# Kernel tuning notes

Measured on AMD Instinct MI355X. Metric: run time of the kernel, lower is better.

Reference implementation:

```python
import jax, jax.numpy as jnp
import numpy as np

H = 16  # number of heads

def setup_inputs() -> dict:
    key = jax.random.key(0)
    ks = jax.random.split(key, 8)
    B, T, D = 4, 2048, 1024
    s = 0.02
    return {
        "query": jax.random.normal(ks[0], (B, T, D), jnp.float32),
        "key":   jax.random.normal(ks[1], (B, T, D), jnp.float32),
        "value": jax.random.normal(ks[2], (B, T, D), jnp.float32),
        "mask":  jnp.ones((B, T, T), jnp.int32),
        # torch nn.Linear weights: [out_features, in_features]
        "Wq": jax.random.normal(ks[3], (D, D), jnp.float32) * s,
        "Wk": jax.random.normal(ks[4], (D, D), jnp.float32) * s,
        "Wv": jax.random.normal(ks[5], (D, D), jnp.float32) * s,
        "Wo": jax.random.normal(ks[6], (D, D), jnp.float32) * s,
        "bo": jnp.zeros((D,), jnp.float32),
    }

def reference(query, key, value, mask, Wq, Wk, Wv, Wo, bo):
    B, Tq, _ = query.shape
    Tk = key.shape[1]
    Dv = Wv.shape[0]
    # linear projections (y = x @ W^T), split into heads: [B, H, T, dh]
    Q = jnp.einsum('btd,ed->bte', query, Wq).reshape(B, Tq, H, -1).transpose(0, 2, 1, 3)
    K = jnp.einsum('btd,ed->bte', key,   Wk).reshape(B, Tk, H, -1).transpose(0, 2, 1, 3)
    V = jnp.einsum('btd,ed->bte', value, Wv).reshape(B, Tk, H, -1).transpose(0, 2, 1, 3)
    d_k = K.shape[-1]
    scores = jnp.einsum('bhqd,bhkd->bhqk', Q, K) / jnp.sqrt(jnp.asarray(d_k, Q.dtype))
    # mask broadcast: [B,1,Tq,Tk]; masked_fill(mask==0, -1e9)
    scores = jnp.where(mask[:, None] == 0, jnp.asarray(-1e9, scores.dtype), scores)
    attn = jax.nn.softmax(scores, axis=-1)
    Z = jnp.einsum('bhqk,bhkd->bhqd', attn, V)          # [B,H,Tq,dh]
    Zc = Z.transpose(0, 2, 1, 3).reshape(B, Tq, Dv)     # concat heads
    return jnp.einsum('btd,ed->bte', Zc, Wo) + bo
```

## Files before the change

kernel.cpp:

```cpp
#include <hip/hip_runtime.h>

typedef __bf16 bf16x8 __attribute__((ext_vector_type(8)));
typedef __bf16 bf16x4 __attribute__((ext_vector_type(4)));
typedef float f32x4 __attribute__((ext_vector_type(4)));
typedef unsigned short u16;
typedef unsigned long long u64;

#define NX 8388608
#define NW 1048576

__device__ __forceinline__ u16 f2bf(float f) {
  union { float f; unsigned u; } c; c.f = f;
  unsigned u = c.u;
  u += 0x7fffu + ((u >> 16) & 1u);
  return (u16)(u >> 16);
}

__device__ __forceinline__ f32x4 mfma16(bf16x8 a, bf16x8 b, f32x4 c) {
  return __builtin_amdgcn_mfma_f32_16x16x32_bf16(a, b, c, 0, 0, 0);
}

__device__ __forceinline__ void gld16(void* lds, const void* g) {
  __builtin_amdgcn_global_load_lds(
      (const __attribute__((address_space(1))) unsigned int*)g,
      (__attribute__((address_space(3))) unsigned int*)lds, 16, 0, 0);
}

__global__ __launch_bounds__(256) void cast_all(
    const float* __restrict__ q, const float* __restrict__ k,
    const float* __restrict__ v, const float* __restrict__ wq,
    const float* __restrict__ wk, const float* __restrict__ wv,
    const float* __restrict__ wo, u16* __restrict__ xbf, u16* __restrict__ wbf,
    const int* __restrict__ mask, u64* __restrict__ bits) {
  if (blockIdx.x >= 14336) {
    const int row = (blockIdx.x - 14336) * 4 + (threadIdx.x >> 6);
    const int lane = threadIdx.x & 63;
    const int* mrow = mask + (long long)row * 2048;
#pragma unroll
    for (int it = 0; it < 32; it++) {
      u64 w = __ballot(mrow[it * 64 + lane] != 0);
      if (lane == 0) bits[row * 32 + it] = w;
    }
    return;
  }
  long long i = ((long long)blockIdx.x * 256 + threadIdx.x) * 8;
  const float* src; u16* dst; long long off;
  if (i < (long long)NX)            { src = q; dst = xbf;            off = i; }
  else if (i < 2LL * NX)            { src = k; dst = xbf + NX;       off = i - NX; }
  else if (i < 3LL * NX)            { src = v; dst = xbf + 2LL * NX; off = i - 2LL * NX; }
  else {
    long long j = i - 3LL * NX;
    int w = (int)(j / NW); off = j - (long long)w * NW;
    src = (w == 0) ? wq : (w == 1) ? wk : (w == 2) ? wv : wo;
    dst = wbf + (long long)w * NW;
  }
  float4 a = *(const float4*)(src + off);
  float4 b = *(const float4*)(src + off + 4);
  u16 o[8] = {f2bf(a.x), f2bf(a.y), f2bf(a.z), f2bf(a.w),
              f2bf(b.x), f2bf(b.y), f2bf(b.z), f2bf(b.w)};
  *(uint4*)(dst + off) = *(const uint4*)o;
}

__device__ __forceinline__ void gstage(
    u16* sAb, u16* sBb, const u16* __restrict__ A, const u16* __restrict__ W,
    int m0, int n0, int k0, int wave, int lr, int gc) {
#pragma unroll
  for (int t = 0; t < 4; t++) {
    const int rb = wave * 32 + t * 8;
    gld16(&sAb[rb * 64], &A[(m0 + rb + lr) * 1024 + k0 + gc * 8]);
    gld16(&sBb[rb * 64], &W[(n0 + rb + lr) * 1024 + k0 + gc * 8]);
  }
}

template <int MODE>
__global__ __launch_bounds__(256, 2) void gemm128(
    const u16* __restrict__ Abase, const u16* __restrict__ Wbase,
    u16* __restrict__ oq, u16* __restrict__ ok, u16* __restrict__ ovt,
    const float* __restrict__ bias, float* __restrict__ of) {
  __shared__ alignas(16) u16 smem[2][2][128 * 64];
  const u16* A = Abase;
  const u16* W = Wbase;
  if (MODE == 0) { A += (long long)blockIdx.z * NX; W += (long long)blockIdx.z * NW; }
  const int tid = threadIdx.x, wave = tid >> 6, lane = tid & 63;
  const int quad = lane >> 4, l15 = lane & 15;
  const int id = blockIdx.y * 8 + blockIdx.x;
  const int id2 = (id & 7) * 64 + (id >> 3);
  const int m0 = (id2 >> 3) * 128, n0 = (id2 & 7) * 128;
  const int wm = (wave & 1) * 64, wn = (wave >> 1) * 64;
  const int lr = lane >> 3;
  const int gc = (lane & 7) ^ lr;
  f32x4 acc[4][4];
#pragma unroll
  for (int i = 0; i < 4; i++)
#pragma unroll
    for (int j = 0; j < 4; j++) acc[i][j] = (f32x4){0.f, 0.f, 0.f, 0.f};

  gstage(smem[0][0], smem[0][1], A, W, m0, n0, 0, wave, lr, gc);
  int buf = 0;
  for (int ks = 0; ks < 16; ks++) {
    if (ks < 15) {
      gstage(smem[buf ^ 1][0], smem[buf ^ 1][1], A, W, m0, n0, (ks + 1) * 64,
             wave, lr, gc);
      asm volatile("s_waitcnt vmcnt(8)" ::: "memory");
    } else {
      asm volatile("s_waitcnt vmcnt(0)" ::: "memory");
    }
    __builtin_amdgcn_s_barrier();
    __builtin_amdgcn_sched_barrier(0);
    const u16* cA = smem[buf][0];
    const u16* cB = smem[buf][1];
#pragma unroll
    for (int kc = 0; kc < 2; kc++) {
      bf16x8 aF[4], bF[4];
#pragma unroll
      for (int i = 0; i < 4; i++)
        aF[i] = *(const bf16x8*)&cA[(wm + 16 * i + l15) * 64 +
                                    (((kc * 4 + quad) ^ (l15 & 7)) * 8)];
#pragma unroll
      for (int j = 0; j < 4; j++)
        bF[j] = *(const bf16x8*)&cB[(wn + 16 * j + l15) * 64 +
                                    (((kc * 4 + quad) ^ (l15 & 7)) * 8)];
#pragma unroll
      for (int i = 0; i < 4; i++)
#pragma unroll
        for (int j = 0; j < 4; j++) acc[i][j] = mfma16(aF[i], bF[j], acc[i][j]);
    }
    __builtin_amdgcn_sched_barrier(0);
    __builtin_amdgcn_s_barrier();
    buf ^= 1;
  }

  if (MODE == 0) {
    const int z = blockIdx.z;
    __syncthreads();
    if (z < 2) {
      const float qscale = (z == 0) ? 0.18033688f : 1.0f;
      u16* dst = (z == 0) ? oq : ok;
      u16* sT = &smem[0][0][0] + wave * 4096;
#pragma unroll
      for (int i = 0; i < 4; i++)
#pragma unroll
        for (int j = 0; j < 4; j++)
#pragma unroll
          for (int r = 0; r < 4; r++) {
            int m = 16 * i + quad * 4 + r;
            int d = 16 * j + l15;
            sT[m * 64 + (((d >> 3) ^ (m & 7)) * 8) + (d & 7)] =
                f2bf(acc[i][j][r] * qscale);
          }
      const int bq = m0 >> 11, t0w = (m0 + wm) & 2047;
      const int hq = (n0 + wn) >> 6;
      u16* dq = dst + ((long long)((bq << 4) + hq) * 2048 + t0w + lane) * 64;
#pragma unroll
      for (int c = 0; c < 8; c++) {
        uint4 val = *(const uint4*)&sT[lane * 64 + ((c ^ (lane & 7)) * 8)];
        *(uint4*)(dq + c * 8) = val;
      }
    } else {
      u16* sT = &smem[0][0][0] + wave * 4096;
#pragma unroll
      for (int i = 0; i < 4; i++)
#pragma unroll
        for (int j = 0; j < 4; j++)
#pragma unroll
          for (int r = 0; r < 4; r++) {
            int m = 16 * i + quad * 4 + r;
            int n = 16 * j + l15;
            sT[n * 64 + (((m >> 3) ^ (n & 7)) * 8) + (m & 7)] = f2bf(acc[i][j][r]);
          }
      const int b = m0 >> 11, t0 = (m0 + wm) & 2047;
      const int h = (n0 + wn) >> 6;
      u16* dst = ovt + ((long long)((b << 4) + h)) * 131072 + lane * 2048 + t0;
#pragma unroll
      for (int c = 0; c < 8; c++) {
        uint4 val = *(const uint4*)&sT[lane * 64 + ((c ^ (lane & 7)) * 8)];
        *(uint4*)(dst + c * 8) = val;
      }
    }
  } else {
    float bb[4];
#pragma unroll
    for (int j = 0; j < 4; j++) bb[j] = bias[n0 + wn + 16 * j + l15];
    __syncthreads();
    float* sW = (float*)&smem[0][0][0] + wave * 2048;
#pragma unroll
    for (int p = 0; p < 2; p++) {
#pragma unroll
      for (int i = 0; i < 4; i++)
#pragma unroll
        for (int jj = 0; jj < 2; jj++)
#pragma unroll
          for (int r = 0; r < 4; r++) {
            int m = 16 * i + quad * 4 + r;
            int d = 16 * jj + l15;
            sW[m * 32 + (((d >> 2) ^ (m & 7)) * 4) + (d & 3)] =
                acc[i][2 * p + jj][r] + bb[2 * p + jj];
          }
      float* dof = of + (long long)(m0 + wm + lane) * 1024 + n0 + wn + p * 32;
#pragma unroll
      for (int c = 0; c < 8; c++) {
        float4 val = *(const float4*)&sW[lane * 32 + ((c ^ (lane & 7)) * 4)];
        *(float4*)(dof + c * 4) = val;
      }
    }
  }
}

__device__ __forceinline__ void stage_tile(
    u16* sKb, u16* sVb, const u16* __restrict__ Kh, const u16* __restrict__ Vt,
    int bh, int kt, int wave, int lr8, int gc8) {
#pragma unroll
  for (int t = 0; t < 2; t++) {
    const int rb = wave * 16 + t * 8;
    const int c = rb + lr8;
    const int kap = (c & 32) + (((c >> 2) & 3) << 3) + ((c & 16) >> 2) + (c & 3);
    gld16(&sKb[rb * 64], &Kh[(bh * 2048 + kt * 64 + kap) * 64 + gc8 * 8]);
    gld16(&sVb[rb * 64], &Vt[(bh * 64 + rb + lr8) * 2048 + kt * 64 + gc8 * 8]);
  }
}

__global__ __launch_bounds__(256, 4) void attn(
    const u16* __restrict__ Qh, const u16* __restrict__ Kh,
    const u16* __restrict__ Vt, const u64* __restrict__ mbits,
    u16* __restrict__ Zc) {
  __shared__ alignas(16) u16 sK[2][64 * 64];
  __shared__ alignas(16) u16 sV[2][64 * 64];
  const int tid = threadIdx.x, wave = tid >> 6, lane = tid & 63;
  const int quad = lane >> 4, l15 = lane & 15;
  const int id = blockIdx.y * 16 + blockIdx.x;
  const int id2 = (id & 7) * 128 + (id >> 3);
  const int bh = id2 >> 4, qt = id2 & 15;
  const int b = bh >> 4, h = bh & 15;
  const int q0 = qt * 128 + wave * 32;
  const int lr8 = lane >> 3, gc8 = (lane & 7) ^ lr8;

  bf16x8 qa[2][2];
#pragma unroll
  for (int g = 0; g < 2; g++)
#pragma unroll
    for (int kc = 0; kc < 2; kc++)
      qa[g][kc] = *(const bf16x8*)&Qh[(bh * 2048 + q0 + g * 16 + l15) * 64 +
                                      kc * 32 + quad * 8];

  const u64* mrow = mbits + (long long)(b * 2048 + q0) * 32;
  u64 am = ~0ull;
#pragma unroll
  for (int i = 0; i < 16; i++) am &= mrow[lane * 16 + i];
  const bool allfull = __all(am == ~0ull);

  f32x4 oacc[2][4];
#pragma unroll
  for (int g = 0; g < 2; g++)
#pragma unroll
    for (int j = 0; j < 4; j++) oacc[g][j] = (f32x4){0.f, 0.f, 0.f, 0.f};
  float lv[2] = {0.f, 0.f};

  stage_tile(&sK[0][0], &sV[0][0], Kh, Vt, bh, 0, wave, lr8, gc8);
  const f32x4 z4 = (f32x4){0.f, 0.f, 0.f, 0.f};

  for (int kt = 0; kt < 32; kt++) {
    const int cur = kt & 1;
    if (kt < 31) {
      stage_tile(&sK[cur ^ 1][0], &sV[cur ^ 1][0], Kh, Vt, bh, kt + 1,
                 wave, lr8, gc8);
      asm volatile("s_waitcnt vmcnt(4)" ::: "memory");
    } else {
      asm volatile("s_waitcnt vmcnt(0)" ::: "memory");
    }
    __builtin_amdgcn_s_barrier();
    __builtin_amdgcn_sched_barrier(0);

    bf16x8 kF[2][4];
#pragma unroll
    for (int kc = 0; kc < 2; kc++)
#pragma unroll
      for (int j = 0; j < 4; j++)
        kF[kc][j] = *(const bf16x8*)&sK[cur][(16 * j + l15) * 64 +
                                            (((kc * 4 + quad) ^ (l15 & 7)) * 8)];
    f32x4 sacc[2][4];
    __builtin_amdgcn_s_setprio(1);
#pragma unroll
    for (int j = 0; j < 4; j++)
#pragma unroll
      for (int g = 0; g < 2; g++) sacc[g][j] = mfma16(kF[0][j], qa[g][0], z4);
#pragma unroll
    for (int j = 0; j < 4; j++)
#pragma unroll
      for (int g = 0; g < 2; g++)
        sacc[g][j] = mfma16(kF[1][j], qa[g][1], sacc[g][j]);
    __builtin_amdgcn_s_setprio(0);

    bf16x8 pa[2][2];
    if (allfull) {
#pragma unroll
      for (int g = 0; g < 2; g++) {
        float ls = 0.f;
#pragma unroll
        for (int kc = 0; kc < 2; kc++) {
          bf16x8 pk;
#pragma unroll
          for (int e = 0; e < 8; e++) {
            float p = __builtin_amdgcn_exp2f(sacc[g][2 * kc + (e >> 2)][e & 3]);
            ls += p;
            pk[e] = (__bf16)p;
          }
          pa[g][kc] = pk;
        }
        lv[g] += ls;
      }
    } else {
#pragma unroll
      for (int g = 0; g < 2; g++) {
        u64 w = mbits[(long long)(b * 2048 + q0 + g * 16 + l15) * 32 + kt];
        float ls = 0.f;
#pragma unroll
        for (int kc = 0; kc < 2; kc++) {
          bf16x8 pk;
#pragma unroll
          for (int e = 0; e < 8; e++) {
            float p = __builtin_amdgcn_exp2f(sacc[g][2 * kc + (e >> 2)][e & 3]);
            p = ((w >> (32 * kc + 8 * quad + e)) & 1ull) ? p : 0.f;
            ls += p;
            pk[e] = (__bf16)p;
          }
          pa[g][kc] = pk;
        }
        lv[g] += ls;
      }
    }

    bf16x8 vF[2][4];
#pragma unroll
    for (int kc = 0; kc < 2; kc++)
#pragma unroll
      for (int j = 0; j < 4; j++)
        vF[kc][j] = *(const bf16x8*)&sV[cur][(16 * j + l15) * 64 +
                                             (((kc * 4 + quad) ^ (l15 & 7)) * 8)];
    __builtin_amdgcn_s_setprio(1);
#pragma unroll
    for (int kc = 0; kc < 2; kc++)
#pragma unroll
      for (int g = 0; g < 2; g++)
#pragma unroll
        for (int j = 0; j < 4; j++)
          oacc[g][j] = mfma16(pa[g][kc], vF[kc][j], oacc[g][j]);
    __builtin_amdgcn_s_setprio(0);
    __builtin_amdgcn_sched_barrier(0);
    __builtin_amdgcn_s_barrier();
  }

#pragma unroll
  for (int g = 0; g < 2; g++) {
    float s = lv[g];
    s += __shfl_xor(s, 16);
    s += __shfl_xor(s, 32);
    float inv[4];
#pragma unroll
    for (int r = 0; r < 4; r++)
      inv[r] = 1.f / __shfl(s, quad * 4 + r);
#pragma unroll
    for (int j = 0; j < 4; j++)
#pragma unroll
      for (int r = 0; r < 4; r++) {
        int t = q0 + g * 16 + quad * 4 + r;
        Zc[(b * 2048 + t) * 1024 + h * 64 + 16 * j + l15] =
            f2bf(oacc[g][j][r] * inv[r]);
      }
  }
}

extern "C" void kernel_launch(void* const* d_in, const int* in_sizes, int n_in,
                              void* d_out, int out_size, void* d_ws, size_t ws_size,
                              hipStream_t stream) {
  (void)in_sizes; (void)n_in; (void)out_size; (void)ws_size;
  const float* q    = (const float*)d_in[0];
  const float* k    = (const float*)d_in[1];
  const float* v    = (const float*)d_in[2];
  const int*   mask = (const int*)d_in[3];
  const float* Wq   = (const float*)d_in[4];
  const float* Wk   = (const float*)d_in[5];
  const float* Wv   = (const float*)d_in[6];
  const float* Wo   = (const float*)d_in[7];
  const float* bo   = (const float*)d_in[8];
  float* out = (float*)d_out;

  u16* Xbf = (u16*)d_ws;
  u16* Wbf = Xbf + 3LL * NX;
  u16* Qh  = Wbf + 4LL * NW;
  u16* Kh  = Qh + (long long)NX;
  u16* Vt  = Kh + (long long)NX;
  u16* Zc  = Vt + (long long)NX;
  u64* Mb  = (u64*)(Zc + (long long)NX);

  cast_all<<<16384, 256, 0, stream>>>(q, k, v, Wq, Wk, Wv, Wo, Xbf, Wbf, mask, Mb);
  gemm128<0><<<dim3(8, 64, 3), 256, 0, stream>>>(Xbf, Wbf, Qh, Kh, Vt, nullptr, nullptr);
  attn<<<dim3(16, 64), 256, 0, stream>>>(Qh, Kh, Vt, Mb, Zc);
  gemm128<1><<<dim3(8, 64), 256, 0, stream>>>(Zc, Wbf + 3LL * NW, nullptr, nullptr, nullptr,
                                              bo, out);
}
```

Baseline: 375.9 us.

## Halve GEMM K-tile for higher occupancy; compute softmax row sums via MFMA

The projection GEMM now stages K-slices of 32 instead of 64, which halves LDS per block. Launch bounds are raised to allow four blocks per CU, and the XOR swizzle and loop count are adjusted to match. This trades more barriers and iterations for more latency hiding through occupancy. Separately, the attention kernel drops the scalar per-lane accumulation of softmax probabilities and the final shuffles. It accumulates row sums with an extra MFMA against a ones vector, shifting VALU work onto the matrix unit at the cost of one more MFMA per chunk.

```diff
diff --git a/kernel.cpp b/kernel.cpp
--- a/kernel.cpp
+++ b/kernel.cpp
@@ -61,23 +61,23 @@
   *(uint4*)(dst + off) = *(const uint4*)o;
 }
 
-__device__ __forceinline__ void gstage(
+__device__ __forceinline__ void gstage32(
     u16* sAb, u16* sBb, const u16* __restrict__ A, const u16* __restrict__ W,
-    int m0, int n0, int k0, int wave, int lr, int gc) {
-#pragma unroll
-  for (int t = 0; t < 4; t++) {
-    const int rb = wave * 32 + t * 8;
-    gld16(&sAb[rb * 64], &A[(m0 + rb + lr) * 1024 + k0 + gc * 8]);
-    gld16(&sBb[rb * 64], &W[(n0 + rb + lr) * 1024 + k0 + gc * 8]);
+    int m0, int n0, int k0, int wave, int lr16, int gc4) {
+#pragma unroll
+  for (int t = 0; t < 2; t++) {
+    const int rb = wave * 32 + t * 16;
+    gld16(&sAb[rb * 32], &A[(m0 + rb + lr16) * 1024 + k0 + gc4 * 8]);
+    gld16(&sBb[rb * 32], &W[(n0 + rb + lr16) * 1024 + k0 + gc4 * 8]);
   }
 }
 
 template <int MODE>
-__global__ __launch_bounds__(256, 2) void gemm128(
+__global__ __launch_bounds__(256, 4) void gemm128(
     const u16* __restrict__ Abase, const u16* __restrict__ Wbase,
     u16* __restrict__ oq, u16* __restrict__ ok, u16* __restrict__ ovt,
     const float* __restrict__ bias, float* __restrict__ of) {
-  __shared__ alignas(16) u16 smem[2][2][128 * 64];
+  __shared__ alignas(16) u16 smem[2][2][128 * 32];
   const u16* A = Abase;
   const u16* W = Wbase;
   if (MODE == 0) { A += (long long)blockIdx.z * NX; W += (long long)blockIdx.z * NW; }
@@ -87,21 +87,22 @@
   const int id2 = (id & 7) * 64 + (id >> 3);
   const int m0 = (id2 >> 3) * 128, n0 = (id2 & 7) * 128;
   const int wm = (wave & 1) * 64, wn = (wave >> 1) * 64;
-  const int lr = lane >> 3;
-  const int gc = (lane & 7) ^ lr;
+  const int lr16 = lane >> 2;
+  const int gc4 = (lane & 3) ^ ((lane >> 3) & 3);
   f32x4 acc[4][4];
 #pragma unroll
   for (int i = 0; i < 4; i++)
 #pragma unroll
     for (int j = 0; j < 4; j++) acc[i][j] = (f32x4){0.f, 0.f, 0.f, 0.f};
 
-  gstage(smem[0][0], smem[0][1], A, W, m0, n0, 0, wave, lr, gc);
+  gstage32(smem[0][0], smem[0][1], A, W, m0, n0, 0, wave, lr16, gc4);
   int buf = 0;
-  for (int ks = 0; ks < 16; ks++) {
-    if (ks < 15) {
-      gstage(smem[buf ^ 1][0], smem[buf ^ 1][1], A, W, m0, n0, (ks + 1) * 64,
-             wave, lr, gc);
-      asm volatile("s_waitcnt vmcnt(8)" ::: "memory");
+  const int cs = (quad ^ ((l15 >> 1) & 3)) * 8;
+  for (int ks = 0; ks < 32; ks++) {
+    if (ks < 31) {
+      gstage32(smem[buf ^ 1][0], smem[buf ^ 1][1], A, W, m0, n0, (ks + 1) * 32,
+               wave, lr16, gc4);
+      asm volatile("s_waitcnt vmcnt(4)" ::: "memory");
     } else {
       asm volatile("s_waitcnt vmcnt(0)" ::: "memory");
     }
@@ -109,22 +110,17 @@
     __builtin_amdgcn_sched_barrier(0);
     const u16* cA = smem[buf][0];
     const u16* cB = smem[buf][1];
-#pragma unroll
-    for (int kc = 0; kc < 2; kc++) {
-      bf16x8 aF[4], bF[4];
-#pragma unroll
-      for (int i = 0; i < 4; i++)
-        aF[i] = *(const bf16x8*)&cA[(wm + 16 * i + l15) * 64 +
-                                    (((kc * 4 + quad) ^ (l15 & 7)) * 8)];
-#pragma unroll
-      for (int j = 0; j < 4; j++)
-        bF[j] = *(const bf16x8*)&cB[(wn + 16 * j + l15) * 64 +
-                                    (((kc * 4 + quad) ^ (l15 & 7)) * 8)];
-#pragma unroll
-      for (int i = 0; i < 4; i++)
-#pragma unroll
-        for (int j = 0; j < 4; j++) acc[i][j] = mfma16(aF[i], bF[j], acc[i][j]);
-    }
+    bf16x8 aF[4], bF[4];
+#pragma unroll
+    for (int i = 0; i < 4; i++)
+      aF[i] = *(const bf16x8*)&cA[(wm + 16 * i + l15) * 32 + cs];
+#pragma unroll
+    for (int j = 0; j < 4; j++)
+      bF[j] = *(const bf16x8*)&cB[(wn + 16 * j + l15) * 32 + cs];
+#pragma unroll
+    for (int i = 0; i < 4; i++)
+#pragma unroll
+      for (int j = 0; j < 4; j++) acc[i][j] = mfma16(aF[i], bF[j], acc[i][j]);
     __builtin_amdgcn_sched_barrier(0);
     __builtin_amdgcn_s_barrier();
     buf ^= 1;
@@ -253,7 +249,12 @@
   for (int g = 0; g < 2; g++)
 #pragma unroll
     for (int j = 0; j < 4; j++) oacc[g][j] = (f32x4){0.f, 0.f, 0.f, 0.f};
-  float lv[2] = {0.f, 0.f};
+  f32x4 lsum[2];
+  lsum[0] = (f32x4){0.f, 0.f, 0.f, 0.f};
+  lsum[1] = (f32x4){0.f, 0.f, 0.f, 0.f};
+  bf16x8 one8;
+#pragma unroll
+  for (int e = 0; e < 8; e++) one8[e] = (__bf16)1.0f;
 
   stage_tile(&sK[0][0], &sV[0][0], Kh, Vt, bh, 0, wave, lr8, gc8);
   const f32x4 z4 = (f32x4){0.f, 0.f, 0.f, 0.f};
@@ -293,39 +294,30 @@
     bf16x8 pa[2][2];
     if (allfull) {
 #pragma unroll
-      for (int g = 0; g < 2; g++) {
-        float ls = 0.f;
+      for (int g = 0; g < 2; g++)
 #pragma unroll
         for (int kc = 0; kc < 2; kc++) {
           bf16x8 pk;
 #pragma unroll
+          for (int e = 0; e < 8; e++)
+            pk[e] = (__bf16)__builtin_amdgcn_exp2f(sacc[g][2 * kc + (e >> 2)][e & 3]);
+          pa[g][kc] = pk;
+        }
+    } else {
+#pragma unroll
+      for (int g = 0; g < 2; g++) {
+        u64 w = mbits[(long long)(b * 2048 + q0 + g * 16 + l15) * 32 + kt];
+#pragma unroll
+        for (int kc = 0; kc < 2; kc++) {
+          bf16x8 pk;
+#pragma unroll
           for (int e = 0; e < 8; e++) {
             float p = __builtin_amdgcn_exp2f(sacc[g][2 * kc + (e >> 2)][e & 3]);
-            ls += p;
+            p = ((w >> (32 * kc + 8 * quad + e)) & 1ull) ? p : 0.f;
             pk[e] = (__bf16)p;
           }
           pa[g][kc] = pk;
         }
-        lv[g] += ls;
-      }
-    } else {
-#pragma unroll
-      for (int g = 0; g < 2; g++) {
-        u64 w = mbits[(long long)(b * 2048 + q0 + g * 16 + l15) * 32 + kt];
-        float ls = 0.f;
-#pragma unroll
-        for (int kc = 0; kc < 2; kc++) {
-          bf16x8 pk;
-#pragma unroll
-          for (int e = 0; e < 8; e++) {
-            float p = __builtin_amdgcn_exp2f(sacc[g][2 * kc + (e >> 2)][e & 3]);
-            p = ((w >> (32 * kc + 8 * quad + e)) & 1ull) ? p : 0.f;
-            ls += p;
-            pk[e] = (__bf16)p;
-          }
-          pa[g][kc] = pk;
-        }
-        lv[g] += ls;
       }
     }
 
@@ -340,10 +332,12 @@
 #pragma unroll
     for (int kc = 0; kc < 2; kc++)
 #pragma unroll
-      for (int g = 0; g < 2; g++)
+      for (int g = 0; g < 2; g++) {
+        lsum[g] = mfma16(pa[g][kc], one8, lsum[g]);
 #pragma unroll
         for (int j = 0; j < 4; j++)
           oacc[g][j] = mfma16(pa[g][kc], vF[kc][j], oacc[g][j]);
+      }
     __builtin_amdgcn_s_setprio(0);
     __builtin_amdgcn_sched_barrier(0);
     __builtin_amdgcn_s_barrier();
@@ -351,13 +345,9 @@
 
 #pragma unroll
   for (int g = 0; g < 2; g++) {
-    float s = lv[g];
-    s += __shfl_xor(s, 16);
-    s += __shfl_xor(s, 32);
     float inv[4];
 #pragma unroll
-    for (int r = 0; r < 4; r++)
-      inv[r] = 1.f / __shfl(s, quad * 4 + r);
+    for (int r = 0; r < 4; r++) inv[r] = 1.f / lsum[g][r];
 #pragma unroll
     for (int j = 0; j < 4; j++)
 #pragma unroll
```

Result: slower. 388.2 us (+3.3%).

## Enlarge projection GEMM tiles to 256x256 with 512 threads

Applied to the files above, without the earlier changes.

Both projection GEMMs now use 256x256 output tiles computed by 8 waves, each holding an 8x4 grid of MFMA accumulators, which raises operand reuse from LDS per loaded byte. The Q/K and output-projection epilogues drop the LDS transpose and write results straight to global memory; only the V transpose still goes through LDS. s_setprio is raised around the MFMA bursts. In exchange the kernel needs 128 KB of LDS per block, so fewer blocks fit per CU. The grid also shrinks to 384 blocks for the QKV projection and 128 for the output projection, which can leave CUs idle. The direct epilogue stores are narrower and less coalesced than the previous vector stores.

```diff
diff --git a/kernel.cpp b/kernel.cpp
--- a/kernel.cpp
+++ b/kernel.cpp
@@ -1,7 +1,6 @@
 #include <hip/hip_runtime.h>
 
 typedef __bf16 bf16x8 __attribute__((ext_vector_type(8)));
-typedef __bf16 bf16x4 __attribute__((ext_vector_type(4)));
 typedef float f32x4 __attribute__((ext_vector_type(4)));
 typedef unsigned short u16;
 typedef unsigned long long u64;
@@ -73,25 +72,25 @@
 }
 
 template <int MODE>
-__global__ __launch_bounds__(256, 2) void gemm128(
+__global__ __launch_bounds__(512, 2) void gemm256(
     const u16* __restrict__ Abase, const u16* __restrict__ Wbase,
     u16* __restrict__ oq, u16* __restrict__ ok, u16* __restrict__ ovt,
     const float* __restrict__ bias, float* __restrict__ of) {
-  __shared__ alignas(16) u16 smem[2][2][128 * 64];
+  __shared__ alignas(16) u16 smem[2][2][256 * 64];
   const u16* A = Abase;
   const u16* W = Wbase;
   if (MODE == 0) { A += (long long)blockIdx.z * NX; W += (long long)blockIdx.z * NW; }
   const int tid = threadIdx.x, wave = tid >> 6, lane = tid & 63;
   const int quad = lane >> 4, l15 = lane & 15;
-  const int id = blockIdx.y * 8 + blockIdx.x;
-  const int id2 = (id & 7) * 64 + (id >> 3);
-  const int m0 = (id2 >> 3) * 128, n0 = (id2 & 7) * 128;
-  const int wm = (wave & 1) * 64, wn = (wave >> 1) * 64;
+  const int id = blockIdx.y * 4 + blockIdx.x;
+  const int id2 = (id & 7) * 16 + (id >> 3);
+  const int m0 = (id2 >> 2) * 256, n0 = (id2 & 3) * 256;
+  const int wm = (wave >> 2) * 128, wn = (wave & 3) * 64;
   const int lr = lane >> 3;
   const int gc = (lane & 7) ^ lr;
-  f32x4 acc[4][4];
-#pragma unroll
-  for (int i = 0; i < 4; i++)
+  f32x4 acc[8][4];
+#pragma unroll
+  for (int i = 0; i < 8; i++)
 #pragma unroll
     for (int j = 0; j < 4; j++) acc[i][j] = (f32x4){0.f, 0.f, 0.f, 0.f};
 
@@ -111,19 +110,21 @@
     const u16* cB = smem[buf][1];
 #pragma unroll
     for (int kc = 0; kc < 2; kc++) {
-      bf16x8 aF[4], bF[4];
-#pragma unroll
-      for (int i = 0; i < 4; i++)
+      bf16x8 aF[8], bF[4];
+#pragma unroll
+      for (int i = 0; i < 8; i++)
         aF[i] = *(const bf16x8*)&cA[(wm + 16 * i + l15) * 64 +
                                     (((kc * 4 + quad) ^ (l15 & 7)) * 8)];
 #pragma unroll
       for (int j = 0; j < 4; j++)
         bF[j] = *(const bf16x8*)&cB[(wn + 16 * j + l15) * 64 +
                                     (((kc * 4 + quad) ^ (l15 & 7)) * 8)];
-#pragma unroll
-      for (int i = 0; i < 4; i++)
+      __builtin_amdgcn_s_setprio(1);
+#pragma unroll
+      for (int i = 0; i < 8; i++)
 #pragma unroll
         for (int j = 0; j < 4; j++) acc[i][j] = mfma16(aF[i], bF[j], acc[i][j]);
+      __builtin_amdgcn_s_setprio(0);
     }
     __builtin_amdgcn_sched_barrier(0);
     __builtin_amdgcn_s_barrier();
@@ -132,77 +133,61 @@
 
   if (MODE == 0) {
     const int z = blockIdx.z;
-    __syncthreads();
     if (z < 2) {
       const float qscale = (z == 0) ? 0.18033688f : 1.0f;
       u16* dst = (z == 0) ? oq : ok;
+#pragma unroll
+      for (int i = 0; i < 8; i++)
+#pragma unroll
+        for (int j = 0; j < 4; j++)
+#pragma unroll
+          for (int r = 0; r < 4; r++) {
+            int m = m0 + wm + 16 * i + quad * 4 + r;
+            int n = n0 + wn + 16 * j + l15;
+            int b = m >> 11, t = m & 2047, h = n >> 6, d = n & 63;
+            dst[(((b << 4) + h) * 2048 + t) * 64 + d] = f2bf(acc[i][j][r] * qscale);
+          }
+    } else {
+      __syncthreads();
       u16* sT = &smem[0][0][0] + wave * 4096;
-#pragma unroll
-      for (int i = 0; i < 4; i++)
-#pragma unroll
-        for (int j = 0; j < 4; j++)
-#pragma unroll
-          for (int r = 0; r < 4; r++) {
-            int m = 16 * i + quad * 4 + r;
-            int d = 16 * j + l15;
-            sT[m * 64 + (((d >> 3) ^ (m & 7)) * 8) + (d & 7)] =
-                f2bf(acc[i][j][r] * qscale);
-          }
-      const int bq = m0 >> 11, t0w = (m0 + wm) & 2047;
-      const int hq = (n0 + wn) >> 6;
-      u16* dq = dst + ((long long)((bq << 4) + hq) * 2048 + t0w + lane) * 64;
-#pragma unroll
-      for (int c = 0; c < 8; c++) {
-        uint4 val = *(const uint4*)&sT[lane * 64 + ((c ^ (lane & 7)) * 8)];
-        *(uint4*)(dq + c * 8) = val;
-      }
-    } else {
-      u16* sT = &smem[0][0][0] + wave * 4096;
-#pragma unroll
-      for (int i = 0; i < 4; i++)
-#pragma unroll
-        for (int j = 0; j < 4; j++)
-#pragma unroll
-          for (int r = 0; r < 4; r++) {
-            int m = 16 * i + quad * 4 + r;
-            int n = 16 * j + l15;
-            sT[n * 64 + (((m >> 3) ^ (n & 7)) * 8) + (m & 7)] = f2bf(acc[i][j][r]);
-          }
-      const int b = m0 >> 11, t0 = (m0 + wm) & 2047;
+      const int b = m0 >> 11;
       const int h = (n0 + wn) >> 6;
-      u16* dst = ovt + ((long long)((b << 4) + h)) * 131072 + lane * 2048 + t0;
-#pragma unroll
-      for (int c = 0; c < 8; c++) {
-        uint4 val = *(const uint4*)&sT[lane * 64 + ((c ^ (lane & 7)) * 8)];
-        *(uint4*)(dst + c * 8) = val;
+#pragma unroll
+      for (int ih = 0; ih < 2; ih++) {
+#pragma unroll
+        for (int i2 = 0; i2 < 4; i2++)
+#pragma unroll
+          for (int j = 0; j < 4; j++)
+#pragma unroll
+            for (int r = 0; r < 4; r++) {
+              int m = 16 * i2 + quad * 4 + r;
+              int n = 16 * j + l15;
+              sT[n * 64 + (((m >> 3) ^ (n & 7)) * 8) + (m & 7)] =
+                  f2bf(acc[ih * 4 + i2][j][r]);
+            }
+        const int t0 = (m0 + wm + ih * 64) & 2047;
+        u16* dstv = ovt + ((long long)((b << 4) + h)) * 131072 + lane * 2048 + t0;
+#pragma unroll
+        for (int c = 0; c < 8; c++) {
+          uint4 val = *(const uint4*)&sT[lane * 64 + ((c ^ (lane & 7)) * 8)];
+          *(uint4*)(dstv + c * 8) = val;
+        }
       }
     }
   } else {
     float bb[4];
 #pragma unroll
     for (int j = 0; j < 4; j++) bb[j] = bias[n0 + wn + 16 * j + l15];
-    __syncthreads();
-    float* sW = (float*)&smem[0][0][0] + wave * 2048;
-#pragma unroll
-    for (int p = 0; p < 2; p++) {
-#pragma unroll
-      for (int i = 0; i < 4; i++)
-#pragma unroll
-        for (int jj = 0; jj < 2; jj++)
-#pragma unroll
-          for (int r = 0; r < 4; r++) {
-            int m = 16 * i + quad * 4 + r;
-            int d = 16 * jj + l15;
-            sW[m * 32 + (((d >> 2) ^ (m & 7)) * 4) + (d & 3)] =
-                acc[i][2 * p + jj][r] + bb[2 * p + jj];
-          }
-      float* dof = of + (long long)(m0 + wm + lane) * 1024 + n0 + wn + p * 32;
-#pragma unroll
-      for (int c = 0; c < 8; c++) {
-        float4 val = *(const float4*)&sW[lane * 32 + ((c ^ (lane & 7)) * 4)];
-        *(float4*)(dof + c * 4) = val;
-      }
-    }
+#pragma unroll
+    for (int i = 0; i < 8; i++)
+#pragma unroll
+      for (int j = 0; j < 4; j++)
+#pragma unroll
+        for (int r = 0; r < 4; r++) {
+          int m = m0 + wm + 16 * i + quad * 4 + r;
+          int n = n0 + wn + 16 * j + l15;
+          of[(long long)m * 1024 + n] = acc[i][j][r] + bb[j];
+        }
   }
 }
 
@@ -393,8 +378,8 @@
   u64* Mb  = (u64*)(Zc + (long long)NX);
 
   cast_all<<<16384, 256, 0, stream>>>(q, k, v, Wq, Wk, Wv, Wo, Xbf, Wbf, mask, Mb);
-  gemm128<0><<<dim3(8, 64, 3), 256, 0, stream>>>(Xbf, Wbf, Qh, Kh, Vt, nullptr, nullptr);
+  gemm256<0><<<dim3(4, 32, 3), 512, 0, stream>>>(Xbf, Wbf, Qh, Kh, Vt, nullptr, nullptr);
   attn<<<dim3(16, 64), 256, 0, stream>>>(Qh, Kh, Vt, Mb, Zc);
-  gemm128<1><<<dim3(8, 64), 256, 0, stream>>>(Zc, Wbf + 3LL * NW, nullptr, nullptr, nullptr,
+  gemm256<1><<<dim3(4, 32), 512, 0, stream>>>(Zc, Wbf + 3LL * NW, nullptr, nullptr, nullptr,
                                               bo, out);
 }
```

Result: slower. 387.5 us (+3.1%).

## Fuse activation fp32-to-bf16 conversion into QKV projection GEMM loads

Applied to the files above, without the earlier changes.

The separate cast kernel no longer converts query/key/value to bf16. Instead the QKV GEMM loads fp32 activation tiles into registers, converts them to bf16 and writes them swizzled into LDS, while weights still use direct global-to-LDS loads. This removes a full write and re-read of the bf16 activation copy. In exchange the GEMM reads twice as many bytes for A, and the register-staged path waits on all loads each iteration, which reduces overlap.

```diff
diff --git a/kernel.cpp b/kernel.cpp
--- a/kernel.cpp
+++ b/kernel.cpp
@@ -1,7 +1,6 @@
 #include <hip/hip_runtime.h>
 
 typedef __bf16 bf16x8 __attribute__((ext_vector_type(8)));
-typedef __bf16 bf16x4 __attribute__((ext_vector_type(4)));
 typedef float f32x4 __attribute__((ext_vector_type(4)));
 typedef unsigned short u16;
 typedef unsigned long long u64;
@@ -26,14 +25,13 @@
       (__attribute__((address_space(3))) unsigned int*)lds, 16, 0, 0);
 }
 
-__global__ __launch_bounds__(256) void cast_all(
-    const float* __restrict__ q, const float* __restrict__ k,
-    const float* __restrict__ v, const float* __restrict__ wq,
-    const float* __restrict__ wk, const float* __restrict__ wv,
-    const float* __restrict__ wo, u16* __restrict__ xbf, u16* __restrict__ wbf,
-    const int* __restrict__ mask, u64* __restrict__ bits) {
-  if (blockIdx.x >= 14336) {
-    const int row = (blockIdx.x - 14336) * 4 + (threadIdx.x >> 6);
+__global__ __launch_bounds__(256) void cast_wm(
+    const float* __restrict__ wq, const float* __restrict__ wk,
+    const float* __restrict__ wv, const float* __restrict__ wo,
+    u16* __restrict__ wbf, const int* __restrict__ mask,
+    u64* __restrict__ bits) {
+  if (blockIdx.x >= 2048) {
+    const int row = (blockIdx.x - 2048) * 4 + (threadIdx.x >> 6);
     const int lane = threadIdx.x & 63;
     const int* mrow = mask + (long long)row * 2048;
 #pragma unroll
@@ -44,16 +42,10 @@
     return;
   }
   long long i = ((long long)blockIdx.x * 256 + threadIdx.x) * 8;
-  const float* src; u16* dst; long long off;
-  if (i < (long long)NX)            { src = q; dst = xbf;            off = i; }
-  else if (i < 2LL * NX)            { src = k; dst = xbf + NX;       off = i - NX; }
-  else if (i < 3LL * NX)            { src = v; dst = xbf + 2LL * NX; off = i - 2LL * NX; }
-  else {
-    long long j = i - 3LL * NX;
-    int w = (int)(j / NW); off = j - (long long)w * NW;
-    src = (w == 0) ? wq : (w == 1) ? wk : (w == 2) ? wv : wo;
-    dst = wbf + (long long)w * NW;
-  }
+  int w = (int)(i / NW);
+  long long off = i - (long long)w * NW;
+  const float* src = (w == 0) ? wq : (w == 1) ? wk : (w == 2) ? wv : wo;
+  u16* dst = wbf + (long long)w * NW;
   float4 a = *(const float4*)(src + off);
   float4 b = *(const float4*)(src + off + 4);
   u16 o[8] = {f2bf(a.x), f2bf(a.y), f2bf(a.z), f2bf(a.w),
@@ -74,13 +66,12 @@
 
 template <int MODE>
 __global__ __launch_bounds__(256, 2) void gemm128(
-    const u16* __restrict__ Abase, const u16* __restrict__ Wbase,
+    const float* __restrict__ Aq, const float* __restrict__ Ak,
+    const float* __restrict__ Av, const u16* __restrict__ Abf,
+    const u16* __restrict__ Wbase,
     u16* __restrict__ oq, u16* __restrict__ ok, u16* __restrict__ ovt,
     const float* __restrict__ bias, float* __restrict__ of) {
   __shared__ alignas(16) u16 smem[2][2][128 * 64];
-  const u16* A = Abase;
-  const u16* W = Wbase;
-  if (MODE == 0) { A += (long long)blockIdx.z * NX; W += (long long)blockIdx.z * NW; }
   const int tid = threadIdx.x, wave = tid >> 6, lane = tid & 63;
   const int quad = lane >> 4, l15 = lane & 15;
   const int id = blockIdx.y * 8 + blockIdx.x;
@@ -89,49 +80,128 @@
   const int wm = (wave & 1) * 64, wn = (wave >> 1) * 64;
   const int lr = lane >> 3;
   const int gc = (lane & 7) ^ lr;
+  const int z = (MODE == 0) ? blockIdx.z : 0;
+  const float* Af = nullptr;
+  const u16* A = nullptr;
+  const u16* W = Wbase;
+  if constexpr (MODE == 0) {
+    Af = (z == 0) ? Aq : (z == 1) ? Ak : Av;
+    W += (long long)z * NW;
+  } else {
+    A = Abf;
+  }
   f32x4 acc[4][4];
 #pragma unroll
   for (int i = 0; i < 4; i++)
 #pragma unroll
     for (int j = 0; j < 4; j++) acc[i][j] = (f32x4){0.f, 0.f, 0.f, 0.f};
 
-  gstage(smem[0][0], smem[0][1], A, W, m0, n0, 0, wave, lr, gc);
-  int buf = 0;
-  for (int ks = 0; ks < 16; ks++) {
-    if (ks < 15) {
-      gstage(smem[buf ^ 1][0], smem[buf ^ 1][1], A, W, m0, n0, (ks + 1) * 64,
-             wave, lr, gc);
-      asm volatile("s_waitcnt vmcnt(8)" ::: "memory");
-    } else {
+  if constexpr (MODE == 0) {
+    float4 ar[4][2];
+#pragma unroll
+    for (int t = 0; t < 4; t++) {
+      const int rb = wave * 32 + t * 8;
+      const float* s = &Af[(long long)(m0 + rb + lr) * 1024 + gc * 8];
+      ar[t][0] = *(const float4*)s;
+      ar[t][1] = *(const float4*)(s + 4);
+    }
+#pragma unroll
+    for (int t = 0; t < 4; t++) {
+      const int rb = wave * 32 + t * 8;
+      gld16(&smem[0][1][rb * 64], &W[(n0 + rb + lr) * 1024 + gc * 8]);
+    }
+    int buf = 0;
+    for (int ks = 0; ks < 16; ks++) {
       asm volatile("s_waitcnt vmcnt(0)" ::: "memory");
-    }
-    __builtin_amdgcn_s_barrier();
-    __builtin_amdgcn_sched_barrier(0);
-    const u16* cA = smem[buf][0];
-    const u16* cB = smem[buf][1];
-#pragma unroll
-    for (int kc = 0; kc < 2; kc++) {
-      bf16x8 aF[4], bF[4];
-#pragma unroll
-      for (int i = 0; i < 4; i++)
-        aF[i] = *(const bf16x8*)&cA[(wm + 16 * i + l15) * 64 +
-                                    (((kc * 4 + quad) ^ (l15 & 7)) * 8)];
-#pragma unroll
-      for (int j = 0; j < 4; j++)
-        bF[j] = *(const bf16x8*)&cB[(wn + 16 * j + l15) * 64 +
-                                    (((kc * 4 + quad) ^ (l15 & 7)) * 8)];
-#pragma unroll
-      for (int i = 0; i < 4; i++)
-#pragma unroll
-        for (int j = 0; j < 4; j++) acc[i][j] = mfma16(aF[i], bF[j], acc[i][j]);
-    }
-    __builtin_amdgcn_sched_barrier(0);
-    __builtin_amdgcn_s_barrier();
-    buf ^= 1;
+      u16* sA = smem[buf][0];
+#pragma unroll
+      for (int t = 0; t < 4; t++) {
+        const int rb = wave * 32 + t * 8;
+        bf16x8 v;
+        v[0] = (__bf16)ar[t][0].x; v[1] = (__bf16)ar[t][0].y;
+        v[2] = (__bf16)ar[t][0].z; v[3] = (__bf16)ar[t][0].w;
+        v[4] = (__bf16)ar[t][1].x; v[5] = (__bf16)ar[t][1].y;
+        v[6] = (__bf16)ar[t][1].z; v[7] = (__bf16)ar[t][1].w;
+        *(bf16x8*)&sA[(rb + lr) * 64 + (lane & 7) * 8] = v;
+      }
+      if (ks < 15) {
+        const int k0 = (ks + 1) * 64;
+#pragma unroll
+        for (int t = 0; t < 4; t++) {
+          const int rb = wave * 32 + t * 8;
+          const float* s = &Af[(long long)(m0 + rb + lr) * 1024 + k0 + gc * 8];
+          ar[t][0] = *(const float4*)s;
+          ar[t][1] = *(const float4*)(s + 4);
+        }
+#pragma unroll
+        for (int t = 0; t < 4; t++) {
+          const int rb = wave * 32 + t * 8;
+          gld16(&smem[buf ^ 1][1][rb * 64], &W[(n0 + rb + lr) * 1024 + k0 + gc * 8]);
+        }
+      }
+      asm volatile("s_waitcnt lgkmcnt(0)" ::: "memory");
+      __builtin_amdgcn_s_barrier();
+      __builtin_amdgcn_sched_barrier(0);
+      const u16* cA = smem[buf][0];
+      const u16* cB = smem[buf][1];
+#pragma unroll
+      for (int kc = 0; kc < 2; kc++) {
+        bf16x8 aF[4], bF[4];
+#pragma unroll
+        for (int i = 0; i < 4; i++)
+          aF[i] = *(const bf16x8*)&cA[(wm + 16 * i + l15) * 64 +
+                                      (((kc * 4 + quad) ^ (l15 & 7)) * 8)];
+#pragma unroll
+        for (int j = 0; j < 4; j++)
+          bF[j] = *(const bf16x8*)&cB[(wn + 16 * j + l15) * 64 +
+                                      (((kc * 4 + quad) ^ (l15 & 7)) * 8)];
+#pragma unroll
+        for (int i = 0; i < 4; i++)
+#pragma unroll
+          for (int j = 0; j < 4; j++) acc[i][j] = mfma16(aF[i], bF[j], acc[i][j]);
+      }
+      __builtin_amdgcn_sched_barrier(0);
+      __builtin_amdgcn_s_barrier();
+      buf ^= 1;
+    }
+  } else {
+    gstage(smem[0][0], smem[0][1], A, W, m0, n0, 0, wave, lr, gc);
+    int buf = 0;
+    for (int ks = 0; ks < 16; ks++) {
+      if (ks < 15) {
+        gstage(smem[buf ^ 1][0], smem[buf ^ 1][1], A, W, m0, n0, (ks + 1) * 64,
+               wave, lr, gc);
+        asm volatile("s_waitcnt vmcnt(8)" ::: "memory");
+      } else {
+        asm volatile("s_waitcnt vmcnt(0)" ::: "memory");
+      }
+      __builtin_amdgcn_s_barrier();
+      __builtin_amdgcn_sched_barrier(0);
+      const u16* cA = smem[buf][0];
+      const u16* cB = smem[buf][1];
+#pragma unroll
+      for (int kc = 0; kc < 2; kc++) {
+        bf16x8 aF[4], bF[4];
+#pragma unroll
+        for (int i = 0; i < 4; i++)
+          aF[i] = *(const bf16x8*)&cA[(wm + 16 * i + l15) * 64 +
+                                      (((kc * 4 + quad) ^ (l15 & 7)) * 8)];
+#pragma unroll
+        for (int j = 0; j < 4; j++)
+          bF[j] = *(const bf16x8*)&cB[(wn + 16 * j + l15) * 64 +
+                                      (((kc * 4 + quad) ^ (l15 & 7)) * 8)];
+#pragma unroll
+        for (int i = 0; i < 4; i++)
+#pragma unroll
+          for (int j = 0; j < 4; j++) acc[i][j] = mfma16(aF[i], bF[j], acc[i][j]);
+      }
+      __builtin_amdgcn_sched_barrier(0);
+      __builtin_amdgcn_s_barrier();
+      buf ^= 1;
+    }
   }
 
   if (MODE == 0) {
-    const int z = blockIdx.z;
     __syncthreads();
     if (z < 2) {
       const float qscale = (z == 0) ? 0.18033688f : 1.0f;
@@ -392,9 +462,11 @@
   u16* Zc  = Vt + (long long)NX;
   u64* Mb  = (u64*)(Zc + (long long)NX);
 
-  cast_all<<<16384, 256, 0, stream>>>(q, k, v, Wq, Wk, Wv, Wo, Xbf, Wbf, mask, Mb);
-  gemm128<0><<<dim3(8, 64, 3), 256, 0, stream>>>(Xbf, Wbf, Qh, Kh, Vt, nullptr, nullptr);
+  cast_wm<<<4096, 256, 0, stream>>>(Wq, Wk, Wv, Wo, Wbf, mask, Mb);
+  gemm128<0><<<dim3(8, 64, 3), 256, 0, stream>>>(q, k, v, nullptr, Wbf,
+                                                 Qh, Kh, Vt, nullptr, nullptr);
   attn<<<dim3(16, 64), 256, 0, stream>>>(Qh, Kh, Vt, Mb, Zc);
-  gemm128<1><<<dim3(8, 64), 256, 0, stream>>>(Zc, Wbf + 3LL * NW, nullptr, nullptr, nullptr,
-                                              bo, out);
-}
+  gemm128<1><<<dim3(8, 64), 256, 0, stream>>>(nullptr, nullptr, nullptr, Zc,
+                                              Wbf + 3LL * NW, nullptr, nullptr,
+                                              nullptr, bo, out);
+}
```

Measured after the change: 398.7 us. +6.1%, slower.
